# Optimization experiments

Hardware: AMD Instinct MI355X
Metric: run time of the kernel (lower is better)

Reference implementation:

```python
import jax, jax.numpy as jnp
import numpy as np
from jax import lax

B, P, W, C = 32, 256, 16, 64
H = 128          # hidden_dim
PRED = 64        # pred_stat_len
TOK = W + 1      # token_len
SIGMA_MIN = 1e-3
EPS = 1e-5


def setup_inputs() -> dict:
    key = jax.random.key(0)
    ks = jax.random.split(key, 20)
    s = 0.05
    inp = {
        "mu_hist": jax.random.normal(ks[0], (B, P, C), jnp.float32),
        "std_hist": jax.random.uniform(ks[1], (B, P, C), jnp.float32, 0.1, 1.5),
        "anchor": jax.random.normal(ks[2], (B, 1, C), jnp.float32),
        "raw_patches": jax.random.normal(ks[3], (B, P, W, C), jnp.float32),
        # mean branch params
        "mean_in_W": jax.random.normal(ks[4], (TOK, H), jnp.float32) * s,
        "mean_in_b": jax.random.normal(ks[5], (H,), jnp.float32) * s,
        "mean_a_logit": jnp.full((H,), float(np.log(9.0)), jnp.float32),
        "mean_post_W": jax.random.normal(ks[6], (H, H), jnp.float32) * s,
        "mean_post_b": jax.random.normal(ks[7], (H,), jnp.float32) * s,
        "mean_out_W": jax.random.normal(ks[8], (H, PRED), jnp.float32) * s,
        "mean_out_b": jax.random.normal(ks[9], (PRED,), jnp.float32) * s,
        "gamma_mu": jax.random.normal(ks[10], (C,), jnp.float32) * s,
        # std branch params
        "std_in_W": jax.random.normal(ks[11], (TOK, H), jnp.float32) * s,
        "std_in_b": jax.random.normal(ks[12], (H,), jnp.float32) * s,
        "std_a_logit": jnp.full((H,), float(np.log(9.0)), jnp.float32),
        "std_post_W": jax.random.normal(ks[13], (H, H), jnp.float32) * s,
        "std_post_b": jax.random.normal(ks[14], (H,), jnp.float32) * s,
        "std_out_W": jax.random.normal(ks[15], (H, PRED), jnp.float32) * s,
        "std_out_b": jax.random.normal(ks[16], (PRED,), jnp.float32) * s,
        "gamma_std": jax.random.normal(ks[17], (C,), jnp.float32) * s,
    }
    return inp


def _ema(u, a_logit):
    # u: (BC, P, H) -> final hidden state (BC, H) via h_t = a*h + (1-a)*u_t
    a = jax.nn.sigmoid(a_logit)
    one_minus_a = 1.0 - a

    def step(h, u_t):
        return a * h + one_minus_a * u_t, None

    h0 = jnp.zeros((u.shape[0], u.shape[2]), u.dtype)
    h, _ = lax.scan(step, h0, jnp.swapaxes(u, 0, 1))  # scan over P
    return h


def _branch(token, in_W, in_b, a_logit, post_W, post_b, out_W, out_b):
    u = token @ in_W + in_b                     # (BC, P, H)
    h = _ema(u, a_logit)                        # (BC, H)
    h = h + jax.nn.gelu(h, approximate=False) @ post_W + post_b
    res = h @ out_W + out_b                     # (BC, PRED)
    return res.reshape(B, C, PRED).transpose(0, 2, 1)  # (B, PRED, C)


def reference(mu_hist, std_hist, anchor, raw_patches,
              mean_in_W, mean_in_b, mean_a_logit, mean_post_W, mean_post_b,
              mean_out_W, mean_out_b, gamma_mu,
              std_in_W, std_in_b, std_a_logit, std_post_W, std_post_b,
              std_out_W, std_out_b, gamma_std):
    BC = B * C
    # --- mean branch ---
    mu_center = mu_hist - anchor                                 # (B,P,C)
    raw_center = raw_patches - anchor[:, :, None, :]             # (B,P,W,C)
    mu_center_t = mu_center.transpose(0, 2, 1).reshape(BC, P, 1)
    raw_center_t = raw_center.transpose(0, 3, 1, 2).reshape(BC, P, W)
    mean_token = jnp.concatenate([mu_center_t, raw_center_t], axis=-1)
    mu_res = _branch(mean_token, mean_in_W, mean_in_b, mean_a_logit,
                     mean_post_W, mean_post_b, mean_out_W, mean_out_b)
    mu_fut = anchor + gamma_mu[None, None, :] * mu_res           # (B,PRED,C)

    # --- std branch ---
    logstd_hist = jnp.log(jnp.maximum(std_hist, SIGMA_MIN))      # (B,P,C)
    logstd_anchor = logstd_hist.mean(axis=1, keepdims=True)      # (B,1,C)
    logstd_center = logstd_hist - logstd_anchor
    z_patch = (raw_patches - mu_hist[:, :, None, :]) / (std_hist[:, :, None, :] + EPS)
    logstd_center_t = logstd_center.transpose(0, 2, 1).reshape(BC, P, 1)
    z_patch_t = z_patch.transpose(0, 3, 1, 2).reshape(BC, P, W)
    std_token = jnp.concatenate([logstd_center_t, z_patch_t], axis=-1)
    logstd_res = _branch(std_token, std_in_W, std_in_b, std_a_logit,
                         std_post_W, std_post_b, std_out_W, std_out_b)
    logstd_fut = logstd_anchor + gamma_std[None, None, :] * logstd_res
    std_fut = jnp.maximum(jnp.exp(logstd_fut), SIGMA_MIN)
    return mu_fut, std_fut
```

## Files before the change

kernel.cpp:

```cpp
#include <hip/hip_runtime.h>
#include <math.h>

#define Bn 32
#define Pn 256
#define Wn 16
#define Cn 64
#define Hn 128
#define PREDn 64
#define TOKn 17
#define TBLK 8

__device__ __forceinline__ void gload_lds(const float* g, float* l) {
  __builtin_amdgcn_global_load_lds(
      (const __attribute__((address_space(1))) unsigned int*)g,
      (__attribute__((address_space(3))) unsigned int*)l, 4, 0, 0);
}

__global__ void lsa_part_kernel(const float* __restrict__ std_hist,
                                float* __restrict__ lsa_part) {
  int b = blockIdx.x;
  int ts = blockIdx.y;
  int c = threadIdx.x & 63;
  int q = threadIdx.x >> 6;
  const float* base = std_hist + ((size_t)b * Pn + ts * 32) * Cn + c;
  float s = 0.f;
#pragma unroll
  for (int i = 0; i < 8; ++i) {
    int t = q + 4 * i;
    s += logf(fmaxf(base[(size_t)t * Cn], 1e-3f));
  }
  __shared__ float red[4][64];
  red[q][c] = s;
  __syncthreads();
  if (q == 0) {
    lsa_part[ts * 2048 + b * 64 + c] = red[0][c] + red[1][c] + red[2][c] + red[3][c];
  }
}

__global__ void lsa_combine_kernel(const float* __restrict__ lsa_part,
                                   float* __restrict__ lsa) {
  int i = blockIdx.x * 256 + threadIdx.x;
  float v = 0.f;
#pragma unroll
  for (int k = 0; k < 8; ++k) v += lsa_part[k * 2048 + i];
  lsa[i] = v * (1.0f / 256.0f);
}

template <int NCH>
__launch_bounds__(256, 2)
__global__ void ema_kernel(
    const float* __restrict__ mu_hist, const float* __restrict__ std_hist,
    const float* __restrict__ raw,
    const float* __restrict__ mW, const float* __restrict__ mal,
    const float* __restrict__ sW, const float* __restrict__ sal,
    float* __restrict__ Spart) {
  constexpr int L = Pn / NCH;
  constexpr int NPH = L / TBLK;
  const int sx = blockIdx.x;
  const int cblk = sx & 1, hblk = (sx >> 1) & 1, ph = sx >> 2;
  const int b = blockIdx.y, br = blockIdx.z;
  const int tid = threadIdx.x;
  const int cr = tid & 31;
  const int w0 = tid >> 5;

  const float* inW = br ? sW : mW;
  const float* alog = br ? sal : mal;
  const int hh0 = hblk * 64 + w0 * 8;

  float Wr[TOKn][8];
#pragma unroll
  for (int k = 0; k < 16; ++k) {
    float4 a0 = *(const float4*)&inW[(1 + k) * Hn + hh0];
    float4 a1 = *(const float4*)&inW[(1 + k) * Hn + hh0 + 4];
    Wr[k][0] = a0.x; Wr[k][1] = a0.y; Wr[k][2] = a0.z; Wr[k][3] = a0.w;
    Wr[k][4] = a1.x; Wr[k][5] = a1.y; Wr[k][6] = a1.z; Wr[k][7] = a1.w;
  }
  {
    float4 a0 = *(const float4*)&inW[hh0];
    float4 a1 = *(const float4*)&inW[hh0 + 4];
    Wr[16][0] = a0.x; Wr[16][1] = a0.y; Wr[16][2] = a0.z; Wr[16][3] = a0.w;
    Wr[16][4] = a1.x; Wr[16][5] = a1.y; Wr[16][6] = a1.z; Wr[16][7] = a1.w;
  }
  float SW[8], av[8], h[8];
#pragma unroll
  for (int i = 0; i < 8; ++i) {
    float s = 0.f;
#pragma unroll
    for (int k = 0; k < 16; ++k) s += Wr[k][i];
    SW[i] = s;
    av[i] = 1.0f / (1.0f + expf(-alog[hh0 + i]));
    h[i] = 0.0f;
  }

  const int chalf = cblk * 32;
  const float* rawb = raw + ((size_t)b * Pn) * (Wn * Cn) + chalf;
  const float* mub = mu_hist + ((size_t)b * Pn) * Cn + chalf;
  const float* sdb = std_hist + ((size_t)b * Pn) * Cn + chalf;

  __shared__ float tokf[2][TBLK][16][32];
  __shared__ float mu_l[2][TBLK][32];
  __shared__ float sd_l[2][TBLK][32];

  const int lane = tid & 63;
  const int wv = tid >> 6;
  const int lw = lane >> 5;
  const int lc = lane & 31;
  const int r0 = wv * 2;
  const int t0 = ph * L;

  auto ISSUE = [&](int tb, int buf) {
#pragma unroll
    for (int rr = 0; rr < 2; ++rr) {
      const int row = r0 + rr;
      const float* gb = rawb + (size_t)(tb + row) * (Wn * Cn);
#pragma unroll
      for (int k = 0; k < 16; k += 2) {
        gload_lds(gb + (k + lw) * Cn + lc, &tokf[buf][row][k][0]);
      }
    }
    gload_lds(mub + (size_t)(tb + r0 + lw) * Cn + lc, &mu_l[buf][r0][0]);
    if (br) gload_lds(sdb + (size_t)(tb + r0 + lw) * Cn + lc, &sd_l[buf][r0][0]);
  };

  auto COMPUTE = [&](int buf) {
#pragma unroll
    for (int r = 0; r < TBLK; ++r) {
      float tk[16];
#pragma unroll
      for (int k = 0; k < 16; ++k) tk[k] = tokf[buf][r][k][cr];
      float sc = mu_l[buf][r][cr];
      if (br == 0) {
#pragma unroll
        for (int i = 0; i < 8; ++i) {
          float u = tk[0] * Wr[0][i];
#pragma unroll
          for (int k = 1; k < 16; ++k) u = fmaf(tk[k], Wr[k][i], u);
          u = fmaf(sc, Wr[16][i], u);
          h[i] = fmaf(av[i], h[i] - u, u);
        }
      } else {
        float sd = sd_l[buf][r][cr];
        float inv = 1.0f / (sd + 1e-5f);
        float ls = logf(fmaxf(sd, 1e-3f));
        float nmi = -sc * inv;
#pragma unroll
        for (int i = 0; i < 8; ++i) {
          float u = tk[0] * Wr[0][i];
#pragma unroll
          for (int k = 1; k < 16; ++k) u = fmaf(tk[k], Wr[k][i], u);
          u = u * inv;
          u = fmaf(nmi, SW[i], u);
          u = fmaf(ls, Wr[16][i], u);
          h[i] = fmaf(av[i], h[i] - u, u);
        }
      }
    }
  };

  ISSUE(t0, 0);
  __syncthreads();
  int cur = 0;
#pragma unroll 1
  for (int p = 0; p < NPH; ++p) {
    if (p + 1 < NPH) ISSUE(t0 + (p + 1) * TBLK, cur ^ 1);
    COMPUTE(cur);
    __syncthreads();
    cur ^= 1;
  }

  const int idx_block = (((br * NCH + ph) * Bn + b) * 2 + cblk) * 2 + hblk;
  float* op = Spart + (size_t)idx_block * 2048 + tid * 8;
  float4 o0 = {h[0], h[1], h[2], h[3]};
  float4 o1 = {h[4], h[5], h[6], h[7]};
  *(float4*)op = o0;
  *(float4*)(op + 4) = o1;
}

template <int G, int NCH>
__launch_bounds__(128, 4)
__global__ void head_kernel(
    const float* __restrict__ anchor, const float* __restrict__ lsa,
    const float* __restrict__ mW, const float* __restrict__ sW,
    const float* __restrict__ mIB, const float* __restrict__ sIB,
    const float* __restrict__ mal, const float* __restrict__ mpW, const float* __restrict__ mpb,
    const float* __restrict__ moW, const float* __restrict__ mob, const float* __restrict__ gmu,
    const float* __restrict__ sal, const float* __restrict__ spW, const float* __restrict__ spb,
    const float* __restrict__ soW, const float* __restrict__ sob, const float* __restrict__ gst,
    const float* __restrict__ Spart, float* __restrict__ out) {
  constexpr int L = Pn / NCH;
  const int br = blockIdx.y;
  const int bc0 = blockIdx.x * G;
  const int tid = threadIdx.x;
  const float* alog = br ? sal : mal;
  const float* pW = br ? spW : mpW;
  const float* pb = br ? spb : mpb;
  const float* oW = br ? soW : moW;
  const float* ob = br ? sob : mob;
  const float inb = br ? sIB[tid] : mIB[tid];

  __shared__ float smem[2 * G * 128];
  float* g_lds = smem;
  float* h2 = smem + G * 128;

  const float a = 1.0f / (1.0f + expf(-alog[tid]));
  float aL = a;
#pragma unroll
  for (int s7 = 0; s7 < 31 - __builtin_clz(L); ++s7) aL *= aL;
  float fac[NCH];
  fac[NCH - 1] = 1.0f;
#pragma unroll
  for (int k = NCH - 2; k >= 0; --k) fac[k] = fac[k + 1] * aL;
  const float apF = fac[0] * aL;
  float SWv;
  if (br == 0) {
    float s = 0.f;
#pragma unroll
    for (int k = 0; k < TOKn; ++k) s += mW[k * Hn + tid];
    SWv = s;
  } else {
    SWv = sW[tid];
  }
  const float om = 1.0f - apF;
  const float cS = om * SWv;

  const int hblk = tid >> 6;
  const int hhg = (tid >> 3) & 7;
  const int ii = tid & 7;

  float hreg[G];
#pragma unroll
  for (int g = 0; g < G; ++g) {
    int bc = bc0 + g;
    int bb = bc >> 6, cc = bc & 63;
    int cblk2 = cc >> 5, crr = cc & 31;
    const size_t inner = (size_t)(hhg * 32 + crr) * 8 + ii;
    const int blk0 = (((br * NCH + 0) * Bn + bb) * 2 + cblk2) * 2 + hblk;
    float hv = 0.f;
#pragma unroll
    for (int k = 0; k < NCH; ++k) {
      hv = fmaf(fac[k], Spart[(size_t)(blk0 + k * (Bn * 4)) * 2048 + inner], hv);
    }
    float shiftv = br ? lsa[bb * Cn + cc] : anchor[bb * Cn + cc];
    hv = fmaf(-cS, shiftv, hv);
    hv = fmaf(om, inb, hv);
    hreg[g] = hv;
    g_lds[g * 128 + tid] = 0.5f * hv * (1.0f + erff(hv * 0.70710678118654752f));
  }
  __syncthreads();

  float acc[G];
#pragma unroll
  for (int g = 0; g < G; ++g) acc[g] = hreg[g] + pb[tid];
  for (int j = 0; j < 128; j += 4) {
    float w0v = pW[j * Hn + tid];
    float w1v = pW[(j + 1) * Hn + tid];
    float w2v = pW[(j + 2) * Hn + tid];
    float w3v = pW[(j + 3) * Hn + tid];
#pragma unroll
    for (int g = 0; g < G; ++g) {
      float4 gv = *(const float4*)&g_lds[g * 128 + j];
      acc[g] = fmaf(gv.x, w0v, acc[g]);
      acc[g] = fmaf(gv.y, w1v, acc[g]);
      acc[g] = fmaf(gv.z, w2v, acc[g]);
      acc[g] = fmaf(gv.w, w3v, acc[g]);
    }
  }
#pragma unroll
  for (int g = 0; g < G; ++g) h2[g * 128 + tid] = acc[g];
  __syncthreads();

  const int p = tid & 63;
  const int jh = tid >> 6;
  float s[G];
#pragma unroll
  for (int g = 0; g < G; ++g) s[g] = 0.f;
  for (int jj = 0; jj < 64; jj += 4) {
    int j = jh * 64 + jj;
    float w0v = oW[j * PREDn + p];
    float w1v = oW[(j + 1) * PREDn + p];
    float w2v = oW[(j + 2) * PREDn + p];
    float w3v = oW[(j + 3) * PREDn + p];
#pragma unroll
    for (int g = 0; g < G; ++g) {
      float4 hv4 = *(const float4*)&h2[g * 128 + j];
      s[g] = fmaf(hv4.x, w0v, s[g]);
      s[g] = fmaf(hv4.y, w1v, s[g]);
      s[g] = fmaf(hv4.z, w2v, s[g]);
      s[g] = fmaf(hv4.w, w3v, s[g]);
    }
  }
  float* red = smem;
#pragma unroll
  for (int g = 0; g < G; ++g) red[jh * (G * 64) + g * 64 + p] = s[g];
  __syncthreads();
  if (tid < 64) {
#pragma unroll
    for (int g = 0; g < G; ++g) {
      int bc = bc0 + g;
      int bb = bc >> 6, cc = bc & 63;
      float tot = red[g * 64 + p] + red[G * 64 + g * 64 + p] + ob[p];
      if (br == 0) {
        out[((size_t)bb * PREDn + p) * Cn + cc] = fmaf(gmu[cc], tot, anchor[bb * Cn + cc]);
      } else {
        float lf = fmaf(gst[cc], tot, lsa[bb * Cn + cc]);
        out[131072 + ((size_t)bb * PREDn + p) * Cn + cc] = fmaxf(expf(lf), 1e-3f);
      }
    }
  }
}

extern "C" void kernel_launch(void* const* d_in, const int* in_sizes, int n_in,
                              void* d_out, int out_size, void* d_ws, size_t ws_size,
                              hipStream_t stream) {
  (void)in_sizes; (void)n_in; (void)out_size;
  const float* mu_hist = (const float*)d_in[0];
  const float* std_hist = (const float*)d_in[1];
  const float* anchor = (const float*)d_in[2];
  const float* raw = (const float*)d_in[3];
  const float* mW = (const float*)d_in[4];
  const float* mb_ = (const float*)d_in[5];
  const float* mal = (const float*)d_in[6];
  const float* mpW = (const float*)d_in[7];
  const float* mpb = (const float*)d_in[8];
  const float* moW = (const float*)d_in[9];
  const float* mob = (const float*)d_in[10];
  const float* gmu = (const float*)d_in[11];
  const float* sW = (const float*)d_in[12];
  const float* sb_ = (const float*)d_in[13];
  const float* sal = (const float*)d_in[14];
  const float* spW = (const float*)d_in[15];
  const float* spb = (const float*)d_in[16];
  const float* soW = (const float*)d_in[17];
  const float* sob = (const float*)d_in[18];
  const float* gst = (const float*)d_in[19];
  float* out = (float*)d_out;
  float* ws = (float*)d_ws;

  float* lsa = ws;
  float* lsa_part = ws + 2048;
  float* Spart = ws + 2048 + 16384;

  const size_t need4 = (size_t)(2048 + 16384 + 1024 * 2048) * 4;

  hipLaunchKernelGGL(lsa_part_kernel, dim3(32, 8), dim3(256), 0, stream, std_hist, lsa_part);
  hipLaunchKernelGGL(lsa_combine_kernel, dim3(8), dim3(256), 0, stream, lsa_part, lsa);
  if (ws_size >= need4) {
    hipLaunchKernelGGL(HIP_KERNEL_NAME(ema_kernel<4>), dim3(16, 32, 2), dim3(256), 0, stream,
                       mu_hist, std_hist, raw, mW, mal, sW, sal, Spart);
    hipLaunchKernelGGL(HIP_KERNEL_NAME(head_kernel<2, 4>), dim3(1024, 2), dim3(128), 0, stream,
                       anchor, lsa, mW, sW, mb_, sb_, mal, mpW, mpb, moW, mob, gmu,
                       sal, spW, spb, soW, sob, gst, Spart, out);
  } else {
    hipLaunchKernelGGL(HIP_KERNEL_NAME(ema_kernel<2>), dim3(8, 32, 2), dim3(256), 0, stream,
                       mu_hist, std_hist, raw, mW, mal, sW, sal, Spart);
    hipLaunchKernelGGL(HIP_KERNEL_NAME(head_kernel<2, 2>), dim3(1024, 2), dim3(128), 0, stream,
                       anchor, lsa, mW, sW, mb_, sb_, mal, mpW, mpb, moW, mob, gmu,
                       sal, spW, spb, soW, sob, gst, Spart, out);
  }
}
```

Baseline: 221.6 us.

## Fuse log-std anchor reduction into head kernel and drop two launches

Removes the two small kernels that computed the per-(b,c) mean of log std, and computes it inside the head kernel's std branch with a wavefront shuffle reduction into shared memory. This cuts two kernel launches and the workspace round trip. In exchange each head block does strided, uncoalesced reads of std_hist and adds a barrier. The ema kernel's launch bounds also drop from 2 to 1 blocks per CU, which lets it use more registers but may lower occupancy.

```diff
diff --git a/kernel.cpp b/kernel.cpp
--- a/kernel.cpp
+++ b/kernel.cpp
@@ -16,38 +16,8 @@
       (__attribute__((address_space(3))) unsigned int*)l, 4, 0, 0);
 }
 
-__global__ void lsa_part_kernel(const float* __restrict__ std_hist,
-                                float* __restrict__ lsa_part) {
-  int b = blockIdx.x;
-  int ts = blockIdx.y;
-  int c = threadIdx.x & 63;
-  int q = threadIdx.x >> 6;
-  const float* base = std_hist + ((size_t)b * Pn + ts * 32) * Cn + c;
-  float s = 0.f;
-#pragma unroll
-  for (int i = 0; i < 8; ++i) {
-    int t = q + 4 * i;
-    s += logf(fmaxf(base[(size_t)t * Cn], 1e-3f));
-  }
-  __shared__ float red[4][64];
-  red[q][c] = s;
-  __syncthreads();
-  if (q == 0) {
-    lsa_part[ts * 2048 + b * 64 + c] = red[0][c] + red[1][c] + red[2][c] + red[3][c];
-  }
-}
-
-__global__ void lsa_combine_kernel(const float* __restrict__ lsa_part,
-                                   float* __restrict__ lsa) {
-  int i = blockIdx.x * 256 + threadIdx.x;
-  float v = 0.f;
-#pragma unroll
-  for (int k = 0; k < 8; ++k) v += lsa_part[k * 2048 + i];
-  lsa[i] = v * (1.0f / 256.0f);
-}
-
 template <int NCH>
-__launch_bounds__(256, 2)
+__launch_bounds__(256, 1)
 __global__ void ema_kernel(
     const float* __restrict__ mu_hist, const float* __restrict__ std_hist,
     const float* __restrict__ raw,
@@ -179,7 +149,7 @@
 template <int G, int NCH>
 __launch_bounds__(128, 4)
 __global__ void head_kernel(
-    const float* __restrict__ anchor, const float* __restrict__ lsa,
+    const float* __restrict__ anchor, const float* __restrict__ std_hist,
     const float* __restrict__ mW, const float* __restrict__ sW,
     const float* __restrict__ mIB, const float* __restrict__ sIB,
     const float* __restrict__ mal, const float* __restrict__ mpW, const float* __restrict__ mpb,
@@ -199,8 +169,26 @@
   const float inb = br ? sIB[tid] : mIB[tid];
 
   __shared__ float smem[2 * G * 128];
+  __shared__ float lsa_sh[G];
   float* g_lds = smem;
   float* h2 = smem + G * 128;
+
+  if (br == 1) {
+    int g = tid >> 6;
+    int lane = tid & 63;
+    int bc = bc0 + g;
+    int bb = bc >> 6, cc = bc & 63;
+    const float* sb = std_hist + (size_t)bb * Pn * Cn + cc;
+    float s = 0.f;
+#pragma unroll
+    for (int i = 0; i < 4; ++i) {
+      s += logf(fmaxf(sb[(size_t)(lane + 64 * i) * Cn], 1e-3f));
+    }
+#pragma unroll
+    for (int off = 32; off; off >>= 1) s += __shfl_down(s, off, 64);
+    if (lane == 0) lsa_sh[g] = s * (1.0f / 256.0f);
+  }
+  __syncthreads();
 
   const float a = 1.0f / (1.0f + expf(-alog[tid]));
   float aL = a;
@@ -240,7 +228,7 @@
     for (int k = 0; k < NCH; ++k) {
       hv = fmaf(fac[k], Spart[(size_t)(blk0 + k * (Bn * 4)) * 2048 + inner], hv);
     }
-    float shiftv = br ? lsa[bb * Cn + cc] : anchor[bb * Cn + cc];
+    float shiftv = br ? lsa_sh[g] : anchor[bb * Cn + cc];
     hv = fmaf(-cS, shiftv, hv);
     hv = fmaf(om, inb, hv);
     hreg[g] = hv;
@@ -302,7 +290,7 @@
       if (br == 0) {
         out[((size_t)bb * PREDn + p) * Cn + cc] = fmaf(gmu[cc], tot, anchor[bb * Cn + cc]);
       } else {
-        float lf = fmaf(gst[cc], tot, lsa[bb * Cn + cc]);
+        float lf = fmaf(gst[cc], tot, lsa_sh[g]);
         out[131072 + ((size_t)bb * PREDn + p) * Cn + cc] = fmaxf(expf(lf), 1e-3f);
       }
     }
@@ -334,27 +322,21 @@
   const float* sob = (const float*)d_in[18];
   const float* gst = (const float*)d_in[19];
   float* out = (float*)d_out;
-  float* ws = (float*)d_ws;
-
-  float* lsa = ws;
-  float* lsa_part = ws + 2048;
-  float* Spart = ws + 2048 + 16384;
-
-  const size_t need4 = (size_t)(2048 + 16384 + 1024 * 2048) * 4;
-
-  hipLaunchKernelGGL(lsa_part_kernel, dim3(32, 8), dim3(256), 0, stream, std_hist, lsa_part);
-  hipLaunchKernelGGL(lsa_combine_kernel, dim3(8), dim3(256), 0, stream, lsa_part, lsa);
+  float* Spart = (float*)d_ws;
+
+  const size_t need4 = (size_t)(1024 * 2048) * 4;
+
   if (ws_size >= need4) {
     hipLaunchKernelGGL(HIP_KERNEL_NAME(ema_kernel<4>), dim3(16, 32, 2), dim3(256), 0, stream,
                        mu_hist, std_hist, raw, mW, mal, sW, sal, Spart);
     hipLaunchKernelGGL(HIP_KERNEL_NAME(head_kernel<2, 4>), dim3(1024, 2), dim3(128), 0, stream,
-                       anchor, lsa, mW, sW, mb_, sb_, mal, mpW, mpb, moW, mob, gmu,
+                       anchor, std_hist, mW, sW, mb_, sb_, mal, mpW, mpb, moW, mob, gmu,
                        sal, spW, spb, soW, sob, gst, Spart, out);
   } else {
     hipLaunchKernelGGL(HIP_KERNEL_NAME(ema_kernel<2>), dim3(8, 32, 2), dim3(256), 0, stream,
                        mu_hist, std_hist, raw, mW, mal, sW, sal, Spart);
     hipLaunchKernelGGL(HIP_KERNEL_NAME(head_kernel<2, 2>), dim3(1024, 2), dim3(128), 0, stream,
-                       anchor, lsa, mW, sW, mb_, sb_, mal, mpW, mpb, moW, mob, gmu,
+                       anchor, std_hist, mW, sW, mb_, sb_, mal, mpW, mpb, moW, mob, gmu,
                        sal, spW, spb, soW, sob, gst, Spart, out);
   }
 }
```

Result: slower. 231.6 us (+4.5%).
